# Kernel tuning notes

Hardware: AMD Instinct MI355X
Metric: run time of the kernel (lower is better)

## Reference

```python
import jax, jax.numpy as jnp
import numpy as np

B, CIN, COUT, H, W_ = 8, 48, 64, 224, 224
KS, PAD = 3, 1
BN_EPS = 1e-5
TWO_PI = 2.0 * np.pi


def _ste(hard, soft):
    # forward value = hard, gradient flows through soft
    return soft + jax.lax.stop_gradient(hard - soft)


def channel_adaptive_bypass(x, out_ch):
    in_ch = x.shape[1]
    repeat, merge = out_ch // in_ch, out_ch % in_ch
    b, _, h, w = x.shape
    parts = []
    if repeat > 0:
        parts.append(jnp.tile(x, (1, repeat, 1, 1)))
    if merge > 0:
        regular = in_ch // merge * (merge - 1)
        parts.append(x[:, :regular].reshape(b, -1, merge - 1, h, w).mean(axis=1))
        parts.append(x[:, regular:].reshape(b, -1, 1, h, w).mean(axis=1))
    return jnp.concatenate(parts, axis=1)


def setup_inputs() -> dict:
    key = jax.random.key(0)
    ks = jax.random.split(key, 2)
    x = jax.random.normal(ks[0], (B, CIN, H, W_), dtype=jnp.float32)
    weight = 0.001 * jax.random.normal(ks[1], (COUT, CIN, KS, KS), dtype=jnp.float32)
    return {
        'x': x,
        'alpha': jnp.ones((1,), jnp.float32),
        'epsilon': jnp.zeros((1, CIN, 1, 1), jnp.float32),
        'tau': jnp.ones((1, CIN, 1, 1), jnp.float32),
        'A': jnp.ones((1, CIN, 1, 1), jnp.float32),
        'weight': weight,
        'gamma': jnp.ones((COUT,), jnp.float32),
        'beta': jnp.zeros((COUT,), jnp.float32),
    }


def reference(x, alpha, epsilon, tau, A, weight, gamma, beta):
    inp = x
    # PeriodicBinarizer: sin-based periodic binarization with tanh STE
    z = (x - epsilon) / tau * TWO_PI
    s = jnp.sin(z)
    xa = _ste(jnp.sign(s), jnp.tanh(s * alpha)) * A
    # BinaryWeightConv2d: per-filter mean-|w| scaled sign weights, clip STE
    scale = jax.lax.stop_gradient(jnp.mean(jnp.abs(weight), axis=(1, 2, 3), keepdims=True))
    bw = _ste(scale * jnp.sign(weight), jnp.clip(weight, -1.0, 1.0))
    y = jax.lax.conv_general_dilated(
        xa, bw, window_strides=(1, 1), padding=((PAD, PAD), (PAD, PAD)),
        dimension_numbers=('NCHW', 'OIHW', 'NCHW'))
    # BatchNorm2d (training mode: batch statistics, biased variance)
    mu = jnp.mean(y, axis=(0, 2, 3), keepdims=True)
    var = jnp.var(y, axis=(0, 2, 3), keepdims=True)
    yn = (y - mu) * jax.lax.rsqrt(var + BN_EPS)
    yn = yn * gamma[None, :, None, None] + beta[None, :, None, None]
    return yn + channel_adaptive_bypass(inp, COUT)
```

## Files before the change

kernel.cpp:

```cpp
#include <hip/hip_runtime.h>
#include <math.h>

#define BB   8
#define CI   48
#define CO   64
#define HH   224
#define WW   224
#define HW   50176
#define NPC  (BB*HW)
#define KWORDS (CO*9)

static_assert(NPC % 256 == 0, "grid exactness");

constexpr float TWO_PI_F = 6.283185307179586476925286766559f;

constexpr size_t YOFF  = 0;
constexpr size_t XBOFF = YOFF  + (size_t)BB*CO*HW*2;
constexpr size_t WBOFF = XBOFF + (size_t)BB*HW*8;
constexpr size_t S2OFF = WBOFF + (size_t)KWORDS*8;
constexpr size_t SAOFF = S2OFF + 64*8;
constexpr size_t S1OFF = SAOFF + 64*4;
constexpr size_t CAOFF = S1OFF + 64*4;
constexpr size_t CBOFF = CAOFF + 64*4;

__global__ void k_prep(const float* __restrict__ w, const float* __restrict__ A,
                       unsigned long long* __restrict__ wb, float* __restrict__ sA,
                       int* __restrict__ S1, unsigned long long* __restrict__ S2) {
    int o = threadIdx.x;
    if (o >= CO) return;
    S1[o] = 0;
    S2[o] = 0ull;
    double acc = 0.0;
    unsigned long long bits[9] = {0,0,0,0,0,0,0,0,0};
    for (int i = 0; i < CI; ++i) {
        #pragma unroll
        for (int k = 0; k < 9; ++k) {
            float wv = w[(size_t)(o*CI + i)*9 + k];
            acc += fabs((double)wv);
            if (wv > 0.0f) bits[k] |= (1ull << i);
        }
    }
    float scale = (float)(acc / 432.0);
    sA[o] = scale * A[0];
    #pragma unroll
    for (int k = 0; k < 9; ++k) wb[o*9 + k] = bits[k];
}

__global__ __launch_bounds__(256) void k_pack(const float* __restrict__ x,
                                              const float* __restrict__ eps,
                                              const float* __restrict__ tau,
                                              unsigned long long* __restrict__ xb) {
    int n = blockIdx.x * 256 + threadIdx.x;
    int b = n / HW, p = n - b * HW;
    const float* xp = x + (size_t)b * CI * HW + p;
    unsigned long long word = 0;
    for (int c = 0; c < CI; ++c) {
        float z = (xp[(size_t)c * HW] - eps[c]) / tau[c] * TWO_PI_F;
        float s = sinf(z);
        if (s > 0.0f) word |= (1ull << c);
    }
    xb[n] = word;
}

#define TW 64
#define TH 4
__global__ __launch_bounds__(256) void k_conv(const unsigned long long* __restrict__ xb,
                                              const unsigned long long* __restrict__ wbg,
                                              short* __restrict__ yint) {
    __shared__ unsigned long long xt[TH + 2][TW + 2];
    __shared__ unsigned long long wbs[KWORDS];
    const int tx = threadIdx.x, ty = threadIdx.y;
    const int tid = ty * TW + tx;
    const int w0 = blockIdx.x * TW, h0 = blockIdx.y * TH, b = blockIdx.z;

    for (int i = tid; i < (TH + 2) * (TW + 2); i += 256) {
        int r = i / (TW + 2), c = i - r * (TW + 2);
        int hh = h0 - 1 + r, ww = w0 - 1 + c;
        unsigned long long v = 0ull;
        if (hh >= 0 && hh < HH && ww >= 0 && ww < WW)
            v = xb[(size_t)(b * HH + hh) * WW + ww];
        xt[r][c] = v;
    }
    for (int i = tid; i < KWORDS; i += 256) wbs[i] = wbg[i];
    __syncthreads();

    const int h = h0 + ty, w = w0 + tx;
    if (w >= WW) return;

    unsigned long long xw[9];
    int msk[9];
    int nv = 0;
    #pragma unroll
    for (int kh = 0; kh < 3; ++kh) {
        const int hh = h - 1 + kh;
        const bool vr = (hh >= 0) && (hh < HH);
        #pragma unroll
        for (int kw = 0; kw < 3; ++kw) {
            const int ww = w - 1 + kw;
            const bool v = vr && (ww >= 0) && (ww < WW);
            const int k = kh * 3 + kw;
            msk[k] = v ? -1 : 0;
            xw[k]  = xt[ty + kh][tx + kw];
            nv    += v ? 1 : 0;
        }
    }

    const size_t obase = (size_t)b * CO * HW + (size_t)h * WW + w;
    for (int o = 0; o < CO; ++o) {
        int pops = 0;
        #pragma unroll
        for (int k = 0; k < 9; ++k) {
            unsigned long long t = xw[k] ^ wbs[o * 9 + k];
            int pc = __popcll(t);
            pops += pc & msk[k];
        }
        int cnt = 48 * nv - 2 * pops;
        yint[obase + (size_t)o * HW] = (short)cnt;
    }
}

__global__ __launch_bounds__(256) void k_stats(const short* __restrict__ yint,
                                               int* __restrict__ S1,
                                               unsigned long long* __restrict__ S2) {
    const int o = blockIdx.x >> 3;
    const int part = blockIdx.x & 7;
    const int tid = threadIdx.x;
    const int t0 = part * 256 + tid;
    int s1 = 0;
    unsigned int s2 = 0;
    for (int b = 0; b < BB; ++b) {
        const short* yp = yint + ((size_t)b * CO + o) * HW;
        for (int p = t0; p < HW; p += 2048) {
            int v = yp[p];
            s1 += v;
            s2 += (unsigned int)(v * v);
        }
    }
    __shared__ long long r1[256];
    __shared__ long long r2[256];
    r1[tid] = s1;
    r2[tid] = (long long)s2;
    __syncthreads();
    for (int st = 128; st > 0; st >>= 1) {
        if (tid < st) { r1[tid] += r1[tid + st]; r2[tid] += r2[tid + st]; }
        __syncthreads();
    }
    if (tid == 0) {
        atomicAdd(&S1[o], (int)r1[0]);
        atomicAdd(&S2[o], (unsigned long long)r2[0]);
    }
}

__global__ void k_coef(const int* __restrict__ S1, const unsigned long long* __restrict__ S2,
                       const float* __restrict__ sA, const float* __restrict__ g,
                       const float* __restrict__ bta, float* __restrict__ cA,
                       float* __restrict__ cB) {
    int o = threadIdx.x;
    if (o >= CO) return;
    double m1 = (double)S1[o] / (double)NPC;
    double m2 = (double)(long long)S2[o] / (double)NPC;
    double var_i = m2 - m1 * m1;
    float s = sA[o];
    float var = (float)((double)s * (double)s * var_i);
    float inv = (float)(1.0 / sqrt((double)var + (double)1e-5f));
    float ca = s * inv * g[o];
    cA[o] = ca;
    cB[o] = bta[o] - (float)(s * m1) * inv * g[o];
}

__global__ __launch_bounds__(256) void k_final(const float* __restrict__ x,
                                               const short* __restrict__ yint,
                                               const float* __restrict__ cA,
                                               const float* __restrict__ cB,
                                               float* __restrict__ out) {
    const int n = blockIdx.x * 256 + threadIdx.x;
    const int b = n / HW, p = n - b * HW;
    const float* xp = x + (size_t)b * CI * HW + p;
    const short* yp = yint + (size_t)b * CO * HW + p;
    float* op = out + (size_t)b * CO * HW + p;

    __shared__ float sA_[CO], sB_[CO];
    if (threadIdx.x < CO) { sA_[threadIdx.x] = cA[threadIdx.x]; sB_[threadIdx.x] = cB[threadIdx.x]; }
    __syncthreads();

    float xc[CI];
    #pragma unroll
    for (int c = 0; c < CI; ++c) xc[c] = xp[(size_t)c * HW];

    #pragma unroll
    for (int o = 0; o < 48; ++o) {
        float yv = (float)yp[(size_t)o * HW];
        op[(size_t)o * HW] = fmaf(sA_[o], yv, sB_[o]) + xc[o];
    }
    #pragma unroll
    for (int j = 0; j < 15; ++j) {
        int o = 48 + j;
        float byp = (xc[j] + xc[j + 15] + xc[j + 30]) * (1.0f / 3.0f);
        float yv = (float)yp[(size_t)o * HW];
        op[(size_t)o * HW] = fmaf(sA_[o], yv, sB_[o]) + byp;
    }
    {
        float byp = (xc[45] + xc[46] + xc[47]) * (1.0f / 3.0f);
        float yv = (float)yp[(size_t)63 * HW];
        op[(size_t)63 * HW] = fmaf(sA_[63], yv, sB_[63]) + byp;
    }
}

extern "C" void kernel_launch(void* const* d_in, const int* in_sizes, int n_in,
                              void* d_out, int out_size, void* d_ws, size_t ws_size,
                              hipStream_t stream) {
    const float* x     = (const float*)d_in[0];
    const float* eps   = (const float*)d_in[2];
    const float* tau   = (const float*)d_in[3];
    const float* A     = (const float*)d_in[4];
    const float* w     = (const float*)d_in[5];
    const float* gamma = (const float*)d_in[6];
    const float* beta  = (const float*)d_in[7];
    float* out = (float*)d_out;

    char* ws = (char*)d_ws;
    short*              yint = (short*)(ws + YOFF);
    unsigned long long* xb   = (unsigned long long*)(ws + XBOFF);
    unsigned long long* wb   = (unsigned long long*)(ws + WBOFF);
    unsigned long long* S2   = (unsigned long long*)(ws + S2OFF);
    float*              sA   = (float*)(ws + SAOFF);
    int*                S1   = (int*)(ws + S1OFF);
    float*              cA   = (float*)(ws + CAOFF);
    float*              cB   = (float*)(ws + CBOFF);

    k_prep <<<1, 64, 0, stream>>>(w, A, wb, sA, S1, S2);
    k_pack <<<NPC / 256, 256, 0, stream>>>(x, eps, tau, xb);
    k_conv <<<dim3((WW + TW - 1) / TW, HH / TH, BB), dim3(TW, TH), 0, stream>>>(xb, wb, yint);
    k_stats<<<CO * 8, 256, 0, stream>>>(yint, S1, S2);
    k_coef <<<1, 64, 0, stream>>>(S1, S2, sA, gamma, beta, cA, cB);
    k_final<<<NPC / 256, 256, 0, stream>>>(x, yint, cA, cB, out);
}
```

Before: 311.7 us.

## Recompute binary conv in stats and final kernels instead of storing int16 output

The int16 conv output buffer is gone. BN statistics are now computed by a kernel that performs the XNOR-popcount conv and reduces sums directly. The final kernel recomputes the conv per pixel pair, with an interior/border specialization, and fuses the BN coefficient computation. Weight packing uses wave ballots across 64 blocks, and packing of x is vectorized with float4. This trades a second pass of popcount compute for removing a large int16 write and read, and for merging the coefficient kernel.

```diff
diff --git a/kernel.cpp b/kernel.cpp
--- a/kernel.cpp
+++ b/kernel.cpp
@@ -1,5 +1,6 @@
 #include <hip/hip_runtime.h>
 #include <math.h>
+#include <type_traits>
 
 #define BB   8
 #define CI   48
@@ -8,202 +9,267 @@
 #define WW   224
 #define HW   50176
 #define NPC  (BB*HW)
-#define KWORDS (CO*9)
-
-static_assert(NPC % 256 == 0, "grid exactness");
+
+typedef unsigned long long u64;
+typedef unsigned int u32;
 
 constexpr float TWO_PI_F = 6.283185307179586476925286766559f;
 
-constexpr size_t YOFF  = 0;
-constexpr size_t XBOFF = YOFF  + (size_t)BB*CO*HW*2;
-constexpr size_t WBOFF = XBOFF + (size_t)BB*HW*8;
-constexpr size_t S2OFF = WBOFF + (size_t)KWORDS*8;
-constexpr size_t SAOFF = S2OFF + 64*8;
-constexpr size_t S1OFF = SAOFF + 64*4;
-constexpr size_t CAOFF = S1OFF + 64*4;
-constexpr size_t CBOFF = CAOFF + 64*4;
-
-__global__ void k_prep(const float* __restrict__ w, const float* __restrict__ A,
-                       unsigned long long* __restrict__ wb, float* __restrict__ sA,
-                       int* __restrict__ S1, unsigned long long* __restrict__ S2) {
-    int o = threadIdx.x;
-    if (o >= CO) return;
-    S1[o] = 0;
-    S2[o] = 0ull;
+constexpr size_t XBOFF = 0;
+constexpr size_t WBOFF = XBOFF + (size_t)NPC * 8;
+constexpr size_t S2OFF = WBOFF + (size_t)CO * 9 * 8;
+constexpr size_t SAOFF = S2OFF + CO * 8;
+constexpr size_t S1OFF = SAOFF + CO * 4;
+
+__global__ __launch_bounds__(64) void k_prep(const float* __restrict__ w,
+                                             const float* __restrict__ A,
+                                             u64* __restrict__ wb, float* __restrict__ sA,
+                                             int* __restrict__ S1, u64* __restrict__ S2) {
+    const int o = blockIdx.x;
+    const int i = threadIdx.x;
+    float wv[9];
     double acc = 0.0;
-    unsigned long long bits[9] = {0,0,0,0,0,0,0,0,0};
-    for (int i = 0; i < CI; ++i) {
+    if (i < CI) {
         #pragma unroll
         for (int k = 0; k < 9; ++k) {
-            float wv = w[(size_t)(o*CI + i)*9 + k];
-            acc += fabs((double)wv);
-            if (wv > 0.0f) bits[k] |= (1ull << i);
-        }
-    }
-    float scale = (float)(acc / 432.0);
-    sA[o] = scale * A[0];
-    #pragma unroll
-    for (int k = 0; k < 9; ++k) wb[o*9 + k] = bits[k];
+            wv[k] = w[(size_t)(o * CI + i) * 9 + k];
+            acc += fabs((double)wv[k]);
+        }
+    } else {
+        #pragma unroll
+        for (int k = 0; k < 9; ++k) wv[k] = 0.0f;
+    }
+    #pragma unroll
+    for (int m = 32; m > 0; m >>= 1) acc += __shfl_xor(acc, m, 64);
+    u64 bits[9];
+    #pragma unroll
+    for (int k = 0; k < 9; ++k) bits[k] = __ballot(i < CI && wv[k] > 0.0f);
+    if (i == 0) {
+        sA[o] = (float)(acc / 432.0) * A[0];
+        S1[o] = 0;
+        S2[o] = 0ull;
+        #pragma unroll
+        for (int k = 0; k < 9; ++k) wb[o * 9 + k] = bits[k];
+    }
 }
 
 __global__ __launch_bounds__(256) void k_pack(const float* __restrict__ x,
                                               const float* __restrict__ eps,
                                               const float* __restrict__ tau,
-                                              unsigned long long* __restrict__ xb) {
-    int n = blockIdx.x * 256 + threadIdx.x;
-    int b = n / HW, p = n - b * HW;
+                                              u64* __restrict__ xb) {
+    const int t = blockIdx.x * 256 + threadIdx.x;
+    const int b = t / (HW / 4);
+    const int r = t - b * (HW / 4);
+    const float4* xp = (const float4*)(x + (size_t)b * CI * HW) + r;
+    u64 w0 = 0, w1 = 0, w2 = 0, w3 = 0;
+    for (int c = 0; c < CI; ++c) {
+        float4 v = xp[(size_t)c * (HW / 4)];
+        const float e = eps[c], tu = tau[c];
+        const u64 bit = 1ull << c;
+        if (sinf((v.x - e) / tu * TWO_PI_F) > 0.0f) w0 |= bit;
+        if (sinf((v.y - e) / tu * TWO_PI_F) > 0.0f) w1 |= bit;
+        if (sinf((v.z - e) / tu * TWO_PI_F) > 0.0f) w2 |= bit;
+        if (sinf((v.w - e) / tu * TWO_PI_F) > 0.0f) w3 |= bit;
+    }
+    ulonglong2* ob = (ulonglong2*)xb + (size_t)t * 2;
+    ob[0] = make_ulonglong2(w0, w1);
+    ob[1] = make_ulonglong2(w2, w3);
+}
+
+__global__ __launch_bounds__(256) void k_stats(const u64* __restrict__ xb,
+                                               const u64* __restrict__ wbg,
+                                               int* __restrict__ S1,
+                                               u64* __restrict__ S2) {
+    __shared__ u64 xw[4][64][9];
+    __shared__ u32 vmask[4][64];
+    __shared__ int r1s[4][64];
+    __shared__ u32 r2s[4][64];
+    const int tid = threadIdx.x;
+    const int wv = tid >> 6;
+    const int lane = tid & 63;
+
+    u64 wl[9];
+    #pragma unroll
+    for (int k = 0; k < 9; ++k) wl[k] = wbg[lane * 9 + k];
+
+    const int tile = blockIdx.x * 4 + wv;
+    const int g = tile * 64 + lane;
+    const int b = g / HW;
+    const int p = g - b * HW;
+    const int h = p / WW;
+    const int w = p - h * WW;
+    u32 m = 0;
+    int nv = 0;
+    #pragma unroll
+    for (int dr = 0; dr < 3; ++dr) {
+        const int hh = h + dr - 1;
+        const bool rv = (hh >= 0) && (hh < HH);
+        #pragma unroll
+        for (int dc = 0; dc < 3; ++dc) {
+            const int ww = w + dc - 1;
+            const bool ok = rv && (ww >= 0) && (ww < WW);
+            const int k = dr * 3 + dc;
+            u64 word = 0;
+            if (ok) { word = xb[(size_t)(b * HH + hh) * WW + ww]; m |= 1u << k; ++nv; }
+            xw[wv][lane][k] = word;
+        }
+    }
+    vmask[wv][lane] = m | ((u32)nv << 12);
+    __syncthreads();
+
+    int s1 = 0;
+    u32 s2 = 0;
+    for (int pl = 0; pl < 64; ++pl) {
+        const u32 mm = vmask[wv][pl];
+        const u64* xx = xw[wv][pl];
+        int pops = 0, cnt;
+        if ((mm & 0x1FFu) == 0x1FFu) {
+            #pragma unroll
+            for (int k = 0; k < 9; ++k) pops += __popcll(xx[k] ^ wl[k]);
+            cnt = 432 - 2 * pops;
+        } else {
+            const int nvp = (int)(mm >> 12);
+            #pragma unroll
+            for (int k = 0; k < 9; ++k) {
+                const int pc = __popcll(xx[k] ^ wl[k]);
+                pops += ((mm >> k) & 1u) ? pc : 0;
+            }
+            cnt = 48 * nvp - 2 * pops;
+        }
+        s1 += cnt;
+        s2 += (u32)(cnt * cnt);
+    }
+    r1s[wv][lane] = s1;
+    r2s[wv][lane] = s2;
+    __syncthreads();
+    if (tid < 64) {
+        const int t1 = r1s[0][tid] + r1s[1][tid] + r1s[2][tid] + r1s[3][tid];
+        const u64 t2 = (u64)r2s[0][tid] + r2s[1][tid] + r2s[2][tid] + r2s[3][tid];
+        atomicAdd(&S1[tid], t1);
+        atomicAdd((unsigned long long*)&S2[tid], t2);
+    }
+}
+
+__global__ __launch_bounds__(256) void k_final(const float* __restrict__ x,
+                                               const u64* __restrict__ xb,
+                                               const u64* __restrict__ wbg,
+                                               const int* __restrict__ S1,
+                                               const u64* __restrict__ S2,
+                                               const float* __restrict__ sA,
+                                               const float* __restrict__ gam,
+                                               const float* __restrict__ bta,
+                                               float* __restrict__ out) {
+    __shared__ u64 wbs[CO * 9];
+    __shared__ float cA[CO], cB[CO];
+    const int tid = threadIdx.x;
+    for (int i = tid; i < CO * 9; i += 256) wbs[i] = wbg[i];
+    if (tid < CO) {
+        const double m1 = (double)S1[tid] / (double)NPC;
+        const double m2 = (double)(long long)S2[tid] / (double)NPC;
+        const double vr = m2 - m1 * m1;
+        const float s = sA[tid];
+        const float var = (float)((double)s * (double)s * vr);
+        const float inv = (float)(1.0 / sqrt((double)var + (double)1e-5f));
+        cA[tid] = s * inv * gam[tid];
+        cB[tid] = bta[tid] - (float)(s * m1) * inv * gam[tid];
+    }
+    __syncthreads();
+
+    const int t = blockIdx.x * 256 + tid;
+    const int gp = t * 2;
+    const int b = gp / HW;
+    const int p = gp - b * HW;
+    const int h = p / WW;
+    const int w = p - h * WW;
+
+    u64 win[3][4];
+    int rok[3], cok[4];
+    #pragma unroll
+    for (int r = 0; r < 3; ++r) { const int hh = h - 1 + r; rok[r] = (hh >= 0 && hh < HH) ? -1 : 0; }
+    #pragma unroll
+    for (int c = 0; c < 4; ++c) { const int ww = w - 1 + c; cok[c] = (ww >= 0 && ww < WW) ? -1 : 0; }
+    const u64* xbb = xb + (size_t)b * HW;
+    #pragma unroll
+    for (int r = 0; r < 3; ++r)
+        #pragma unroll
+        for (int c = 0; c < 4; ++c)
+            win[r][c] = (rok[r] & cok[c]) ? xbb[(h - 1 + r) * WW + (w - 1 + c)] : 0ull;
+
+    int nv0 = 0, nv1 = 0;
+    #pragma unroll
+    for (int r = 0; r < 3; ++r)
+        #pragma unroll
+        for (int ck = 0; ck < 3; ++ck) {
+            nv0 += (rok[r] & cok[ck]) ? 1 : 0;
+            nv1 += (rok[r] & cok[ck + 1]) ? 1 : 0;
+        }
+    const bool inter = (rok[0] & rok[1] & rok[2] & cok[0] & cok[3]) != 0;
+
     const float* xp = x + (size_t)b * CI * HW + p;
-    unsigned long long word = 0;
-    for (int c = 0; c < CI; ++c) {
-        float z = (xp[(size_t)c * HW] - eps[c]) / tau[c] * TWO_PI_F;
-        float s = sinf(z);
-        if (s > 0.0f) word |= (1ull << c);
-    }
-    xb[n] = word;
-}
-
-#define TW 64
-#define TH 4
-__global__ __launch_bounds__(256) void k_conv(const unsigned long long* __restrict__ xb,
-                                              const unsigned long long* __restrict__ wbg,
-                                              short* __restrict__ yint) {
-    __shared__ unsigned long long xt[TH + 2][TW + 2];
-    __shared__ unsigned long long wbs[KWORDS];
-    const int tx = threadIdx.x, ty = threadIdx.y;
-    const int tid = ty * TW + tx;
-    const int w0 = blockIdx.x * TW, h0 = blockIdx.y * TH, b = blockIdx.z;
-
-    for (int i = tid; i < (TH + 2) * (TW + 2); i += 256) {
-        int r = i / (TW + 2), c = i - r * (TW + 2);
-        int hh = h0 - 1 + r, ww = w0 - 1 + c;
-        unsigned long long v = 0ull;
-        if (hh >= 0 && hh < HH && ww >= 0 && ww < WW)
-            v = xb[(size_t)(b * HH + hh) * WW + ww];
-        xt[r][c] = v;
-    }
-    for (int i = tid; i < KWORDS; i += 256) wbs[i] = wbg[i];
-    __syncthreads();
-
-    const int h = h0 + ty, w = w0 + tx;
-    if (w >= WW) return;
-
-    unsigned long long xw[9];
-    int msk[9];
-    int nv = 0;
-    #pragma unroll
-    for (int kh = 0; kh < 3; ++kh) {
-        const int hh = h - 1 + kh;
-        const bool vr = (hh >= 0) && (hh < HH);
-        #pragma unroll
-        for (int kw = 0; kw < 3; ++kw) {
-            const int ww = w - 1 + kw;
-            const bool v = vr && (ww >= 0) && (ww < WW);
-            const int k = kh * 3 + kw;
-            msk[k] = v ? -1 : 0;
-            xw[k]  = xt[ty + kh][tx + kw];
-            nv    += v ? 1 : 0;
-        }
-    }
-
-    const size_t obase = (size_t)b * CO * HW + (size_t)h * WW + w;
-    for (int o = 0; o < CO; ++o) {
-        int pops = 0;
-        #pragma unroll
-        for (int k = 0; k < 9; ++k) {
-            unsigned long long t = xw[k] ^ wbs[o * 9 + k];
-            int pc = __popcll(t);
-            pops += pc & msk[k];
-        }
-        int cnt = 48 * nv - 2 * pops;
-        yint[obase + (size_t)o * HW] = (short)cnt;
-    }
-}
-
-__global__ __launch_bounds__(256) void k_stats(const short* __restrict__ yint,
-                                               int* __restrict__ S1,
-                                               unsigned long long* __restrict__ S2) {
-    const int o = blockIdx.x >> 3;
-    const int part = blockIdx.x & 7;
-    const int tid = threadIdx.x;
-    const int t0 = part * 256 + tid;
-    int s1 = 0;
-    unsigned int s2 = 0;
-    for (int b = 0; b < BB; ++b) {
-        const short* yp = yint + ((size_t)b * CO + o) * HW;
-        for (int p = t0; p < HW; p += 2048) {
-            int v = yp[p];
-            s1 += v;
-            s2 += (unsigned int)(v * v);
-        }
-    }
-    __shared__ long long r1[256];
-    __shared__ long long r2[256];
-    r1[tid] = s1;
-    r2[tid] = (long long)s2;
-    __syncthreads();
-    for (int st = 128; st > 0; st >>= 1) {
-        if (tid < st) { r1[tid] += r1[tid + st]; r2[tid] += r2[tid + st]; }
-        __syncthreads();
-    }
-    if (tid == 0) {
-        atomicAdd(&S1[o], (int)r1[0]);
-        atomicAdd(&S2[o], (unsigned long long)r2[0]);
-    }
-}
-
-__global__ void k_coef(const int* __restrict__ S1, const unsigned long long* __restrict__ S2,
-                       const float* __restrict__ sA, const float* __restrict__ g,
-                       const float* __restrict__ bta, float* __restrict__ cA,
-                       float* __restrict__ cB) {
-    int o = threadIdx.x;
-    if (o >= CO) return;
-    double m1 = (double)S1[o] / (double)NPC;
-    double m2 = (double)(long long)S2[o] / (double)NPC;
-    double var_i = m2 - m1 * m1;
-    float s = sA[o];
-    float var = (float)((double)s * (double)s * var_i);
-    float inv = (float)(1.0 / sqrt((double)var + (double)1e-5f));
-    float ca = s * inv * g[o];
-    cA[o] = ca;
-    cB[o] = bta[o] - (float)(s * m1) * inv * g[o];
-}
-
-__global__ __launch_bounds__(256) void k_final(const float* __restrict__ x,
-                                               const short* __restrict__ yint,
-                                               const float* __restrict__ cA,
-                                               const float* __restrict__ cB,
-                                               float* __restrict__ out) {
-    const int n = blockIdx.x * 256 + threadIdx.x;
-    const int b = n / HW, p = n - b * HW;
-    const float* xp = x + (size_t)b * CI * HW + p;
-    const short* yp = yint + (size_t)b * CO * HW + p;
     float* op = out + (size_t)b * CO * HW + p;
 
-    __shared__ float sA_[CO], sB_[CO];
-    if (threadIdx.x < CO) { sA_[threadIdx.x] = cA[threadIdx.x]; sB_[threadIdx.x] = cB[threadIdx.x]; }
-    __syncthreads();
-
-    float xc[CI];
-    #pragma unroll
-    for (int c = 0; c < CI; ++c) xc[c] = xp[(size_t)c * HW];
-
-    #pragma unroll
-    for (int o = 0; o < 48; ++o) {
-        float yv = (float)yp[(size_t)o * HW];
-        op[(size_t)o * HW] = fmaf(sA_[o], yv, sB_[o]) + xc[o];
-    }
-    #pragma unroll
-    for (int j = 0; j < 15; ++j) {
-        int o = 48 + j;
-        float byp = (xc[j] + xc[j + 15] + xc[j + 30]) * (1.0f / 3.0f);
-        float yv = (float)yp[(size_t)o * HW];
-        op[(size_t)o * HW] = fmaf(sA_[o], yv, sB_[o]) + byp;
-    }
-    {
-        float byp = (xc[45] + xc[46] + xc[47]) * (1.0f / 3.0f);
-        float yv = (float)yp[(size_t)63 * HW];
-        op[(size_t)63 * HW] = fmaf(sA_[63], yv, sB_[63]) + byp;
-    }
+    auto run = [&](auto INTER) {
+        constexpr bool IN = decltype(INTER)::value;
+        for (int o = 0; o < CI; ++o) {
+            const u64* wo = &wbs[o * 9];
+            int p0 = 0, p1 = 0;
+            #pragma unroll
+            for (int r = 0; r < 3; ++r)
+                #pragma unroll
+                for (int ck = 0; ck < 3; ++ck) {
+                    const u64 wvv = wo[r * 3 + ck];
+                    const int a = __popcll(win[r][ck] ^ wvv);
+                    const int bq = __popcll(win[r][ck + 1] ^ wvv);
+                    if (IN) { p0 += a; p1 += bq; }
+                    else {
+                        p0 += (rok[r] & cok[ck]) ? a : 0;
+                        p1 += (rok[r] & cok[ck + 1]) ? bq : 0;
+                    }
+                }
+            const int cnt0 = (IN ? 432 : 48 * nv0) - 2 * p0;
+            const int cnt1 = (IN ? 432 : 48 * nv1) - 2 * p1;
+            const float a0 = cA[o], b0 = cB[o];
+            const float2 xv = *(const float2*)(xp + (size_t)o * HW);
+            *(float2*)(op + (size_t)o * HW) =
+                make_float2(fmaf(a0, (float)cnt0, b0) + xv.x,
+                            fmaf(a0, (float)cnt1, b0) + xv.y);
+        }
+        #pragma unroll
+        for (int j = 0; j < 16; ++j) {
+            const int o = CI + j;
+            const u64* wo = &wbs[o * 9];
+            int p0 = 0, p1 = 0;
+            #pragma unroll
+            for (int r = 0; r < 3; ++r)
+                #pragma unroll
+                for (int ck = 0; ck < 3; ++ck) {
+                    const u64 wvv = wo[r * 3 + ck];
+                    const int a = __popcll(win[r][ck] ^ wvv);
+                    const int bq = __popcll(win[r][ck + 1] ^ wvv);
+                    if (IN) { p0 += a; p1 += bq; }
+                    else {
+                        p0 += (rok[r] & cok[ck]) ? a : 0;
+                        p1 += (rok[r] & cok[ck + 1]) ? bq : 0;
+                    }
+                }
+            const int cnt0 = (IN ? 432 : 48 * nv0) - 2 * p0;
+            const int cnt1 = (IN ? 432 : 48 * nv1) - 2 * p1;
+            const float a0 = cA[o], b0 = cB[o];
+            const int c0 = (j < 15) ? j      : 45;
+            const int c1 = (j < 15) ? j + 15 : 46;
+            const int c2 = (j < 15) ? j + 30 : 47;
+            const float2 xv0 = *(const float2*)(xp + (size_t)c0 * HW);
+            const float2 xv1 = *(const float2*)(xp + (size_t)c1 * HW);
+            const float2 xv2 = *(const float2*)(xp + (size_t)c2 * HW);
+            const float bx = (xv0.x + xv1.x + xv2.x) * (1.0f / 3.0f);
+            const float by = (xv0.y + xv1.y + xv2.y) * (1.0f / 3.0f);
+            *(float2*)(op + (size_t)o * HW) =
+                make_float2(fmaf(a0, (float)cnt0, b0) + bx,
+                            fmaf(a0, (float)cnt1, b0) + by);
+        }
+    };
+    if (inter) run(std::true_type{});
+    else       run(std::false_type{});
 }
 
 extern "C" void kernel_launch(void* const* d_in, const int* in_sizes, int n_in,
@@ -219,19 +285,14 @@
     float* out = (float*)d_out;
 
     char* ws = (char*)d_ws;
-    short*              yint = (short*)(ws + YOFF);
-    unsigned long long* xb   = (unsigned long long*)(ws + XBOFF);
-    unsigned long long* wb   = (unsigned long long*)(ws + WBOFF);
-    unsigned long long* S2   = (unsigned long long*)(ws + S2OFF);
-    float*              sA   = (float*)(ws + SAOFF);
-    int*                S1   = (int*)(ws + S1OFF);
-    float*              cA   = (float*)(ws + CAOFF);
-    float*              cB   = (float*)(ws + CBOFF);
-
-    k_prep <<<1, 64, 0, stream>>>(w, A, wb, sA, S1, S2);
-    k_pack <<<NPC / 256, 256, 0, stream>>>(x, eps, tau, xb);
-    k_conv <<<dim3((WW + TW - 1) / TW, HH / TH, BB), dim3(TW, TH), 0, stream>>>(xb, wb, yint);
-    k_stats<<<CO * 8, 256, 0, stream>>>(yint, S1, S2);
-    k_coef <<<1, 64, 0, stream>>>(S1, S2, sA, gamma, beta, cA, cB);
-    k_final<<<NPC / 256, 256, 0, stream>>>(x, yint, cA, cB, out);
-}
+    u64*   xb = (u64*)(ws + XBOFF);
+    u64*   wb = (u64*)(ws + WBOFF);
+    u64*   S2 = (u64*)(ws + S2OFF);
+    float* sA = (float*)(ws + SAOFF);
+    int*   S1 = (int*)(ws + S1OFF);
+
+    k_prep <<<CO, 64, 0, stream>>>(w, A, wb, sA, S1, S2);
+    k_pack <<<NPC / 4 / 256, 256, 0, stream>>>(x, eps, tau, xb);
+    k_stats<<<NPC / 64 / 4, 256, 0, stream>>>(xb, wb, S1, S2);
+    k_final<<<NPC / 2 / 256, 256, 0, stream>>>(x, xb, wb, S1, S2, sA, gamma, beta, out);
+}
```

Measured after the change: 361.4 us. +16.0%, slower.
